# Kernel optimization log

Measured on AMD Instinct MI355X. Metric: run time of the kernel, lower is better.

## Reference

```python
import jax, jax.numpy as jnp
import numpy as np


def setup_inputs() -> dict:
    key = jax.random.key(0)
    k1, k2 = jax.random.split(key)
    B, C, L = 64, 36, 4096
    x0 = jax.random.normal(k1, (B, C, L), dtype=jnp.float32)
    y0 = jax.random.normal(k2, (B, C, L), dtype=jnp.float32)
    return {"x0": x0, "y0": y0}


def reference(x0, y0):
    # Original torch code:
    #   result1 = (1/L) * sum_{i=0}^{L-1} roll(x0, i, dim=2) * y0
    #   result2 = (1/L) * sum_{i=0}^{L-1} roll(y0, i, dim=2) * y0
    # At each output position l, summing roll(x,i)[...,l] over all L shifts
    # visits every position of x exactly once, so the shift-sum equals the
    # full sum over the last axis. The loop is therefore mathematically
    # identical to:
    #   result1 = y0 * mean(x0, axis=-1, keepdims=True)
    #   result2 = y0 * mean(y0, axis=-1, keepdims=True)
    # which we compute in one fused pass (bit-for-bit same math up to
    # floating-point summation order).
    mean_x = jnp.mean(x0, axis=-1, keepdims=True)  # [B,C,1]
    mean_y = jnp.mean(y0, axis=-1, keepdims=True)  # [B,C,1]
    result = y0 * (mean_x + mean_y)                # [B,C,L]
    return result
```

## Files before the change

### kernel.cpp

```cpp
#include <hip/hip_runtime.h>
#include <stdint.h>


#define LL    4096
#define ROWS  (64 * 36)
#define BLOCK 256

__global__ __launch_bounds__(BLOCK) void spo2_rowscale(
    const float* __restrict__ x,
    const float* __restrict__ y,
    float* __restrict__ out)
{
    const int row = blockIdx.x;
    const size_t base = (size_t)row * LL;
    const int tid = threadIdx.x;

    const float4* xv = (const float4*)(x + base);
    const float4* yv = (const float4*)(y + base);
    float4*       ov = (float4*)(out + base);

    float4 xr[4], yr[4];
#pragma unroll
    for (int i = 0; i < 4; ++i) {
        xr[i] = xv[tid + i * BLOCK];
        yr[i] = yv[tid + i * BLOCK];
    }

    float s = 0.f;
#pragma unroll
    for (int i = 0; i < 4; ++i) {
        s += xr[i].x + xr[i].y + xr[i].z + xr[i].w;
        s += yr[i].x + yr[i].y + yr[i].z + yr[i].w;
    }

#pragma unroll
    for (int off = 32; off > 0; off >>= 1)
        s += __shfl_down(s, off, 64);

    __shared__ float rs[BLOCK / 64];
    const int wid  = tid >> 6;
    const int lane = tid & 63;
    if (lane == 0) rs[wid] = s;
    __syncthreads();

    float total = 0.f;
#pragma unroll
    for (int w = 0; w < BLOCK / 64; ++w) total += rs[w];
    const float scale = total * (1.0f / (float)LL);

#pragma unroll
    for (int i = 0; i < 4; ++i) {
        float4 o;
        o.x = yr[i].x * scale;
        o.y = yr[i].y * scale;
        o.z = yr[i].z * scale;
        o.w = yr[i].w * scale;
        ov[tid + i * BLOCK] = o;
    }
}

extern "C" void kernel_launch(void* const* d_in, const int* in_sizes, int n_in,
                              void* d_out, int out_size, void* d_ws, size_t ws_size,
                              hipStream_t stream) {
    const float* x = (const float*)d_in[0];
    const float* y = (const float*)d_in[1];
    float* out = (float*)d_out;
    spo2_rowscale<<<ROWS, BLOCK, 0, stream>>>(x, y, out);
}
```

Baseline: 107.1 us.

## Assign one wavefront per row and use nontemporal output stores

Each 64-lane wavefront now reduces and scales a whole row, so the row sum needs only a wave-level xor shuffle and no shared memory or block barrier. Each lane holds 16 float4 of y in registers and accumulates partial sums into four independent accumulators. Output writes use nontemporal stores so they bypass cache retention. The cost is higher register pressure (64 floats of y per lane), which can lower occupancy and latency hiding, and only 576 blocks are launched.

```diff
diff --git a/kernel.cpp b/kernel.cpp
--- a/kernel.cpp
+++ b/kernel.cpp
@@ -4,58 +4,52 @@
 
 #define LL    4096
 #define ROWS  (64 * 36)
-#define BLOCK 256
+#define WPB   4
+#define NV    16
 
-__global__ __launch_bounds__(BLOCK) void spo2_rowscale(
+typedef float v4f __attribute__((ext_vector_type(4)));
+
+__global__ __launch_bounds__(256) void spo2_waverow(
     const float* __restrict__ x,
     const float* __restrict__ y,
     float* __restrict__ out)
 {
-    const int row = blockIdx.x;
-    const size_t base = (size_t)row * LL;
-    const int tid = threadIdx.x;
+    const int wave = blockIdx.x * WPB + (threadIdx.x >> 6);
+    const int lane = threadIdx.x & 63;
+    const size_t base = (size_t)wave * LL;
 
     const float4* xv = (const float4*)(x + base);
     const float4* yv = (const float4*)(y + base);
-    float4*       ov = (float4*)(out + base);
+    v4f*          ov = (v4f*)(out + base);
 
-    float4 xr[4], yr[4];
+    float4 yr[NV];
+    float s0 = 0.f, s1 = 0.f, s2 = 0.f, s3 = 0.f;
 #pragma unroll
-    for (int i = 0; i < 4; ++i) {
-        xr[i] = xv[tid + i * BLOCK];
-        yr[i] = yv[tid + i * BLOCK];
+    for (int i = 0; i < NV; ++i) {
+        float4 xc = xv[lane + i * 64];
+        float4 yc = yv[lane + i * 64];
+        yr[i] = yc;
+        s0 += xc.x + xc.y;
+        s1 += xc.z + xc.w;
+        s2 += yc.x + yc.y;
+        s3 += yc.z + yc.w;
     }
-
-    float s = 0.f;
-#pragma unroll
-    for (int i = 0; i < 4; ++i) {
-        s += xr[i].x + xr[i].y + xr[i].z + xr[i].w;
-        s += yr[i].x + yr[i].y + yr[i].z + yr[i].w;
-    }
+    float s = (s0 + s1) + (s2 + s3);
 
 #pragma unroll
     for (int off = 32; off > 0; off >>= 1)
-        s += __shfl_down(s, off, 64);
+        s += __shfl_xor(s, off, 64);
 
-    __shared__ float rs[BLOCK / 64];
-    const int wid  = tid >> 6;
-    const int lane = tid & 63;
-    if (lane == 0) rs[wid] = s;
-    __syncthreads();
-
-    float total = 0.f;
-#pragma unroll
-    for (int w = 0; w < BLOCK / 64; ++w) total += rs[w];
-    const float scale = total * (1.0f / (float)LL);
+    const float scale = s * (1.0f / (float)LL);
 
 #pragma unroll
-    for (int i = 0; i < 4; ++i) {
-        float4 o;
+    for (int i = 0; i < NV; ++i) {
+        v4f o;
         o.x = yr[i].x * scale;
         o.y = yr[i].y * scale;
         o.z = yr[i].z * scale;
         o.w = yr[i].w * scale;
-        ov[tid + i * BLOCK] = o;
+        __builtin_nontemporal_store(o, &ov[lane + i * 64]);
     }
 }
 
@@ -65,5 +59,5 @@
     const float* x = (const float*)d_in[0];
     const float* y = (const float*)d_in[1];
     float* out = (float*)d_out;
-    spo2_rowscale<<<ROWS, BLOCK, 0, stream>>>(x, y, out);
+    spo2_waverow<<<ROWS / WPB, 256, 0, stream>>>(x, y, out);
 }
```

After: 107.2 us. No clear change (+0.1%).
